# Optimization experiments

Measured on AMD Instinct MI355X. Metric: run time of the kernel, lower is better.

Reference implementation:

```python
import jax, jax.numpy as jnp
import numpy as np

NUM_GROUPS1 = 8
NUM_GROUPS2 = 4
NUM_HEADS = 8


def setup_inputs() -> dict:
    key = jax.random.key(0)
    k1, k2, k3 = jax.random.split(key, 3)
    B, N, C = 8, 4096, 512
    x = jax.random.normal(k1, (B, N, C), dtype=jnp.float32)
    # torch Linear(dim, 3*inner_dim, bias=False); stored transposed for x @ W
    W_qkv = jax.random.normal(k2, (C, 3 * C), dtype=jnp.float32) * 0.02
    W_proj = jax.random.normal(k3, (C, C), dtype=jnp.float32) * 0.02
    b_proj = jnp.zeros((C,), dtype=jnp.float32)
    return {"x": x, "W_qkv": W_qkv, "W_proj": W_proj, "b_proj": b_proj,
            "recursive_index": 0}


def reference(x, W_qkv, W_proj, b_proj, recursive_index):
    # recursive_index is a static Python int (0 -> False branch, num_groups1).
    num_groups = NUM_GROUPS1 if not recursive_index else NUM_GROUPS2
    B, N, C = x.shape
    H = NUM_HEADS
    Dh = C // H
    scale = Dh ** -0.5
    Np = int(np.ceil(N / num_groups) * num_groups)
    if Np != N:
        x = jnp.pad(x, ((0, 0), (0, Np - N), (0, 0)))
    L = Np // num_groups  # tokens per group
    # qkv projection, then split into per-group per-head tensors [B,G,H,L,Dh]
    qkv = (x @ W_qkv).reshape(B, num_groups, L, 3, H, Dh)
    q = jnp.transpose(qkv[:, :, :, 0], (0, 1, 3, 2, 4))
    k = jnp.transpose(qkv[:, :, :, 1], (0, 1, 3, 2, 4))
    v = jnp.transpose(qkv[:, :, :, 2], (0, 1, 3, 2, 4))
    attn = jax.nn.softmax(jnp.einsum('bghld,bghmd->bghlm', q, k) * scale, axis=-1)
    out = jnp.einsum('bghlm,bghmd->bghld', attn, v)  # [B,G,H,L,Dh]
    out = jnp.transpose(out, (0, 1, 3, 2, 4)).reshape(B, Np, C)[:, :N]
    return out @ W_proj + b_proj
```

## Files before the change

### kernel.cpp

```cpp
#include <hip/hip_runtime.h>
#include <hip/hip_bf16.h>

typedef __attribute__((ext_vector_type(8))) short  bf16x8;
typedef __attribute__((ext_vector_type(4))) float  f32x4;

__device__ __forceinline__ ushort f2bf(float f) {
    unsigned u = __builtin_bit_cast(unsigned, f);
    u += 0x7fffu + ((u >> 16) & 1u);
    return (ushort)(u >> 16);
}

__device__ __forceinline__ void gload_lds16(const ushort* g, ushort* l) {
    __builtin_amdgcn_global_load_lds(
        (const __attribute__((address_space(1))) void*)(g),
        (__attribute__((address_space(3))) void*)(l), 16, 0, 0);
}

__global__ __launch_bounds__(256) void cvt_bf16_kernel(
        const float* __restrict__ in, ushort* __restrict__ out, int n4) {
    int i = blockIdx.x * 256 + threadIdx.x;
    if (i >= n4) return;
    float4 f = reinterpret_cast<const float4*>(in)[i];
    ushort4 o;
    o.x = f2bf(f.x); o.y = f2bf(f.y); o.z = f2bf(f.z); o.w = f2bf(f.w);
    reinterpret_cast<ushort4*>(out)[i] = o;
}

__global__ __launch_bounds__(256) void transpose_cvt_kernel(
        const float* __restrict__ in, ushort* __restrict__ out,
        int Cc, int qcols, float qscale) {
    __shared__ ushort t[64 * 65];
    const int cBase = blockIdx.x * 64, rBase = blockIdx.y * 64;
#pragma unroll
    for (int p = 0; p < 16; ++p) {
        int lin = p * 256 + threadIdx.x;
        int r = lin >> 6, c = lin & 63;
        float v = in[(size_t)(rBase + r) * Cc + cBase + c];
        if (cBase + c < qcols) v *= qscale;
        t[c * 65 + r] = f2bf(v);
    }
    __syncthreads();
#pragma unroll
    for (int p = 0; p < 16; ++p) {
        int lin = p * 256 + threadIdx.x;
        int c = lin >> 6, r = lin & 63;
        out[(size_t)(cBase + c) * 512 + rBase + r] = t[c * 65 + r];
    }
}

template<bool F32OUT, bool EMIT_VT>
__global__ __launch_bounds__(256) void gemm_bt_kernel(
        const ushort* __restrict__ A, const ushort* __restrict__ Bt,
        void* __restrict__ Cout, const float* __restrict__ bias,
        ushort* __restrict__ vT, int Ncols, int K) {
    __shared__ ushort smem[8704];
    ushort* la = smem;
    ushort* lb = smem + 4096;
    const int tid  = threadIdx.x;
    const int mBase = blockIdx.y << 7, nBase = blockIdx.x << 7;
    const int w = tid >> 6, lane = tid & 63, ml = lane & 15, quad = lane >> 4;
    const int wr = (w >> 1) << 6, wc = (w & 1) << 6;

    const int srow   = lane >> 2;
    const int schunk = (lane & 3) ^ (srow & 3) ^ ((srow >> 2) & 3);
    const ushort* Ap = A + (size_t)(mBase + w * 32 + srow) * K + schunk * 8;
    const ushort* Bp = Bt + (size_t)(nBase + w * 32 + srow) * K + schunk * 8;
    ushort* lA0 = la + (w * 32) * 32;
    ushort* lB0 = lb + (w * 32) * 32;

    f32x4 z4 = {0.f, 0.f, 0.f, 0.f};
    f32x4 acc[4][4];
#pragma unroll
    for (int i = 0; i < 4; ++i)
#pragma unroll
        for (int j = 0; j < 4; ++j) acc[i][j] = z4;

    const int sx = ((quad ^ (ml & 3) ^ ((ml >> 2) & 3)) << 3);
    const int nkt = K >> 5;
    for (int kt = 0; kt < nkt; ++kt) {
        gload_lds16(Ap,          lA0);
        gload_lds16(Ap + 16 * K, lA0 + 16 * 32);
        gload_lds16(Bp,          lB0);
        gload_lds16(Bp + 16 * K, lB0 + 16 * 32);
        Ap += 32; Bp += 32;
        __syncthreads();
        bf16x8 af[4], bv[4];
#pragma unroll
        for (int i = 0; i < 4; ++i)
            af[i] = *reinterpret_cast<bf16x8*>(la + (wr + i * 16 + ml) * 32 + sx);
#pragma unroll
        for (int j = 0; j < 4; ++j)
            bv[j] = *reinterpret_cast<bf16x8*>(lb + (wc + j * 16 + ml) * 32 + sx);
#pragma unroll
        for (int i = 0; i < 4; ++i)
#pragma unroll
            for (int j = 0; j < 4; ++j)
                acc[i][j] = __builtin_amdgcn_mfma_f32_16x16x32_bf16(af[i], bv[j], acc[i][j], 0, 0, 0);
        __syncthreads();
    }

    if (F32OUT) {
        float* ep = reinterpret_cast<float*>(smem) + w * 1088;
        float bj[4];
#pragma unroll
        for (int j = 0; j < 4; ++j) bj[j] = bias[nBase + wc + j * 16 + ml];
        float* cbase = reinterpret_cast<float*>(Cout);
#pragma unroll
        for (int i = 0; i < 4; ++i) {
#pragma unroll
            for (int j = 0; j < 4; ++j)
#pragma unroll
                for (int r = 0; r < 4; ++r)
                    ep[(quad * 4 + r) * 68 + j * 16 + ml] = acc[i][j][r] + bj[j];
#pragma unroll
            for (int t = 0; t < 4; ++t) {
                int ch = quad + 4 * t;
                float4 v = *reinterpret_cast<const float4*>(ep + ml * 68 + ch * 4);
                *reinterpret_cast<float4*>(cbase
                    + (size_t)(mBase + wr + i * 16 + ml) * Ncols + nBase + wc + ch * 4) = v;
            }
        }
    } else {
        ushort* ep = smem + w * 1152;
        const bool vblk = EMIT_VT && (nBase >= 1024);
#pragma unroll
        for (int i = 0; i < 4; ++i) {
#pragma unroll
            for (int j = 0; j < 4; ++j)
#pragma unroll
                for (int r = 0; r < 4; ++r)
                    ep[(quad * 4 + r) * 72 + j * 16 + ml] = f2bf(acc[i][j][r]);
            if (!vblk) {
#pragma unroll
                for (int t = 0; t < 2; ++t) {
                    int ch = quad + 4 * t;
                    bf16x8 v = *reinterpret_cast<const bf16x8*>(ep + ml * 72 + ch * 8);
                    *reinterpret_cast<bf16x8*>(reinterpret_cast<ushort*>(Cout)
                        + (size_t)(mBase + wr + i * 16 + ml) * Ncols + nBase + wc + ch * 8) = v;
                }
            } else {
#pragma unroll
                for (int t = 0; t < 2; ++t) {
                    bf16x8 p;
#pragma unroll
                    for (int k = 0; k < 8; ++k)
                        p[k] = (short)ep[(t * 8 + k) * 72 + lane];
                    int tok = mBase + wr + i * 16 + t * 8;
                    int vg  = (nBase - 1024) + wc + lane;
                    *reinterpret_cast<bf16x8*>(vT
                        + ((size_t)((tok >> 9) * 512 + vg)) * 512 + (tok & 511)) = p;
                }
            }
        }
    }
}

__global__ __launch_bounds__(256) void attn_kernel(
        const ushort* __restrict__ qk, const ushort* __restrict__ vT,
        ushort* __restrict__ out) {
    __shared__ ushort k_lds[32 * 64];
    __shared__ ushort v_lds[64 * 32];
    __shared__ ushort p_lds[4 * 32 * 40];
    const int tid = threadIdx.x;
    const int w = tid >> 6, lane = tid & 63, ml = lane & 15, quad = lane >> 4;
    const int id = blockIdx.x;
    const int bgh = id >> 2, qc = id & 3;
    const int b = bgh >> 6, g = (bgh >> 3) & 7, h = bgh & 7;
    const int tb = b * 4096 + g * 512;
    const ushort* base  = qk + (size_t)tb * 1024 + h * 64;
    const ushort* vbase = vT + ((size_t)((b * 8 + g) * 512 + h * 64)) * 512;
    const int qOff = qc * 128 + w * 32;

    bf16x8 qf[2][2];
#pragma unroll
    for (int qb = 0; qb < 2; ++qb)
#pragma unroll
        for (int ks = 0; ks < 2; ++ks)
            qf[qb][ks] = *reinterpret_cast<const bf16x8*>(
                base + (size_t)(qOff + qb * 16 + ml) * 1024 + ks * 32 + quad * 8);

    const int krl = lane >> 3;
    const int kch = (lane & 7) ^ krl;
    const ushort* kp = base + (size_t)(w * 8 + krl) * 1024 + 512 + kch * 8;
    ushort* kdst = k_lds + (w * 8) * 64;
    const int vrl = lane >> 2;
    const int vch = (lane & 3) ^ (vrl & 3) ^ ((vrl >> 2) & 3);
    const ushort* vp = vbase + (size_t)(w * 16 + vrl) * 512 + vch * 8;
    ushort* vdst = v_lds + (w * 16) * 32;

    f32x4 z4 = {0.f, 0.f, 0.f, 0.f};
    f32x4 oacc[2][4];
    float lp[2][4];
#pragma unroll
    for (int qb = 0; qb < 2; ++qb) {
#pragma unroll
        for (int db = 0; db < 4; ++db) oacc[qb][db] = z4;
#pragma unroll
        for (int r = 0; r < 4; ++r) lp[qb][r] = 0.f;
    }

    const int ksw = ml & 7;
    const int vsw = (ml & 3) ^ ((ml >> 2) & 3);
    ushort* pw = p_lds + w * 32 * 40;
    for (int kt = 0; kt < 16; ++kt) {
        gload_lds16(kp + (size_t)kt * 32 * 1024, kdst);
        gload_lds16(vp + kt * 32, vdst);
        __syncthreads();

        bf16x8 kf[2][2];
#pragma unroll
        for (int kb = 0; kb < 2; ++kb)
#pragma unroll
            for (int ks = 0; ks < 2; ++ks)
                kf[kb][ks] = *reinterpret_cast<bf16x8*>(
                    k_lds + (kb * 16 + ml) * 64 + (((ks * 4 + quad) ^ ksw) << 3));
        f32x4 s[2][2];
#pragma unroll
        for (int qb = 0; qb < 2; ++qb)
#pragma unroll
            for (int kb = 0; kb < 2; ++kb) {
                f32x4 t = z4;
                t = __builtin_amdgcn_mfma_f32_16x16x32_bf16(qf[qb][0], kf[kb][0], t, 0, 0, 0);
                t = __builtin_amdgcn_mfma_f32_16x16x32_bf16(qf[qb][1], kf[kb][1], t, 0, 0, 0);
                s[qb][kb] = t;
            }

#pragma unroll
        for (int qb = 0; qb < 2; ++qb)
#pragma unroll
            for (int r = 0; r < 4; ++r) {
                float p0 = exp2f(s[qb][0][r]);
                float p1 = exp2f(s[qb][1][r]);
                lp[qb][r] += p0 + p1;
                pw[(qb * 16 + quad * 4 + r) * 40 + ml]      = f2bf(p0);
                pw[(qb * 16 + quad * 4 + r) * 40 + 16 + ml] = f2bf(p1);
            }

        bf16x8 pf[2], vf[4];
#pragma unroll
        for (int qb = 0; qb < 2; ++qb)
            pf[qb] = *reinterpret_cast<bf16x8*>(pw + (qb * 16 + ml) * 40 + quad * 8);
#pragma unroll
        for (int db = 0; db < 4; ++db)
            vf[db] = *reinterpret_cast<bf16x8*>(
                v_lds + (db * 16 + ml) * 32 + ((quad ^ vsw) << 3));
#pragma unroll
        for (int qb = 0; qb < 2; ++qb)
#pragma unroll
            for (int db = 0; db < 4; ++db)
                oacc[qb][db] = __builtin_amdgcn_mfma_f32_16x16x32_bf16(pf[qb], vf[db], oacc[qb][db], 0, 0, 0);
        __syncthreads();
    }

#pragma unroll
    for (int qb = 0; qb < 2; ++qb) {
        float inv[4];
#pragma unroll
        for (int r = 0; r < 4; ++r) {
            float sline = lp[qb][r];
            sline += __shfl_xor(sline, 1);
            sline += __shfl_xor(sline, 2);
            sline += __shfl_xor(sline, 4);
            sline += __shfl_xor(sline, 8);
            inv[r] = 1.0f / sline;
        }
#pragma unroll
        for (int db = 0; db < 4; ++db)
#pragma unroll
            for (int r = 0; r < 4; ++r) {
                float v = oacc[qb][db][r] * inv[r];
                out[(size_t)(tb + qOff + qb * 16 + quad * 4 + r) * 512
                    + h * 64 + db * 16 + ml] = f2bf(v);
            }
    }
}

extern "C" void kernel_launch(void* const* d_in, const int* in_sizes, int n_in,
                              void* d_out, int out_size, void* d_ws, size_t ws_size,
                              hipStream_t stream) {
    const float* x     = (const float*)d_in[0];
    const float* Wqkv  = (const float*)d_in[1];
    const float* Wproj = (const float*)d_in[2];
    const float* bproj = (const float*)d_in[3];

    char* ws = (char*)d_ws;
    ushort* xb   = (ushort*)(ws);
    ushort* wq   = (ushort*)(ws + 33554432);
    ushort* wp   = (ushort*)(ws + 35127296);
    ushort* qkb  = (ushort*)(ws + 35651584);
    ushort* vTb  = (ushort*)(ws + 102760448);
    ushort* attn = xb;
    float*  outp = (float*)d_out;

    cvt_bf16_kernel<<<16384, 256, 0, stream>>>(x, xb, 4194304);
    transpose_cvt_kernel<<<dim3(24, 8), 256, 0, stream>>>(
        Wqkv, wq, 1536, 512, 0.18033688011112043f);
    transpose_cvt_kernel<<<dim3(8, 8), 256, 0, stream>>>(Wproj, wp, 512, 0, 1.0f);
    gemm_bt_kernel<false, true><<<dim3(12, 256), 256, 0, stream>>>(
        xb, wq, qkb, nullptr, vTb, 1024, 512);
    attn_kernel<<<2048, 256, 0, stream>>>(qkb, vTb, attn);
    gemm_bt_kernel<true, false><<<dim3(4, 256), 256, 0, stream>>>(
        attn, wp, outp, bproj, nullptr, 512, 512);
}
```

Measured before the change: 328.0 us.

## Fuse prep kernels, swizzle GEMM tiles, coalesce vT stores, transpose attention scores

Merges the x conversion and both weight transpose/convert launches into one prep kernel, which removes two launches. The GEMM grid becomes 1D with an XCD-aware mapping so neighbouring M tiles share an N column. The V-transpose epilogue now stages a full 64x64 tile in LDS per wave pair and writes contiguous 16-byte token rows instead of scattered 8-element gathers. In attention, the QK MFMA operands are swapped so each lane holds four keys of one query. P can then be stored as packed ushort4 and the row sums need fewer shuffles, at the cost of extra __syncthreads in the vT epilogue.

```diff
diff --git a/kernel.cpp b/kernel.cpp
--- a/kernel.cpp
+++ b/kernel.cpp
@@ -16,35 +16,45 @@
         (__attribute__((address_space(3))) void*)(l), 16, 0, 0);
 }
 
-__global__ __launch_bounds__(256) void cvt_bf16_kernel(
-        const float* __restrict__ in, ushort* __restrict__ out, int n4) {
-    int i = blockIdx.x * 256 + threadIdx.x;
-    if (i >= n4) return;
-    float4 f = reinterpret_cast<const float4*>(in)[i];
-    ushort4 o;
-    o.x = f2bf(f.x); o.y = f2bf(f.y); o.z = f2bf(f.z); o.w = f2bf(f.w);
-    reinterpret_cast<ushort4*>(out)[i] = o;
-}
-
-__global__ __launch_bounds__(256) void transpose_cvt_kernel(
-        const float* __restrict__ in, ushort* __restrict__ out,
-        int Cc, int qcols, float qscale) {
+__global__ __launch_bounds__(256) void prep_kernel(
+        const float* __restrict__ x, ushort* __restrict__ xb,
+        const float* __restrict__ Wqkv, ushort* __restrict__ wq,
+        const float* __restrict__ Wproj, ushort* __restrict__ wp) {
     __shared__ ushort t[64 * 65];
-    const int cBase = blockIdx.x * 64, rBase = blockIdx.y * 64;
+    const int bx = blockIdx.x, tid = threadIdx.x;
+    if (bx < 16384) {
+        int i = bx * 256 + tid;
+        float4 f = reinterpret_cast<const float4*>(x)[i];
+        ushort4 o;
+        o.x = f2bf(f.x); o.y = f2bf(f.y); o.z = f2bf(f.z); o.w = f2bf(f.w);
+        reinterpret_cast<ushort4*>(xb)[i] = o;
+        return;
+    }
+    const float* in; ushort* out; int Cc, qcols, cB, rB; float qs;
+    if (bx < 16576) {
+        int b2 = bx - 16384;
+        in = Wqkv; out = wq; Cc = 1536; qcols = 512;
+        qs = 0.18033688011112043f;
+        cB = (b2 % 24) * 64; rB = (b2 / 24) * 64;
+    } else {
+        int b2 = bx - 16576;
+        in = Wproj; out = wp; Cc = 512; qcols = 0; qs = 1.0f;
+        cB = (b2 % 8) * 64; rB = (b2 / 8) * 64;
+    }
 #pragma unroll
     for (int p = 0; p < 16; ++p) {
-        int lin = p * 256 + threadIdx.x;
+        int lin = p * 256 + tid;
         int r = lin >> 6, c = lin & 63;
-        float v = in[(size_t)(rBase + r) * Cc + cBase + c];
-        if (cBase + c < qcols) v *= qscale;
+        float v = in[(size_t)(rB + r) * Cc + cB + c];
+        if (cB + c < qcols) v *= qs;
         t[c * 65 + r] = f2bf(v);
     }
     __syncthreads();
 #pragma unroll
     for (int p = 0; p < 16; ++p) {
-        int lin = p * 256 + threadIdx.x;
+        int lin = p * 256 + tid;
         int c = lin >> 6, r = lin & 63;
-        out[(size_t)(cBase + c) * 512 + rBase + r] = t[c * 65 + r];
+        out[(size_t)(cB + c) * 512 + rB + r] = t[c * 65 + r];
     }
 }
 
@@ -53,11 +63,13 @@
         const ushort* __restrict__ A, const ushort* __restrict__ Bt,
         void* __restrict__ Cout, const float* __restrict__ bias,
         ushort* __restrict__ vT, int Ncols, int K) {
-    __shared__ ushort smem[8704];
+    __shared__ ushort smem[9216];
     ushort* la = smem;
     ushort* lb = smem + 4096;
     const int tid  = threadIdx.x;
-    const int mBase = blockIdx.y << 7, nBase = blockIdx.x << 7;
+    const int id = blockIdx.x;
+    const int mBase = ((id & 7) * 32 + ((id >> 3) & 31)) << 7;
+    const int nBase = (id >> 8) << 7;
     const int w = tid >> 6, lane = tid & 63, ml = lane & 15, quad = lane >> 4;
     const int wr = (w >> 1) << 6, wc = (w & 1) << 6;
 
@@ -120,9 +132,8 @@
                     + (size_t)(mBase + wr + i * 16 + ml) * Ncols + nBase + wc + ch * 4) = v;
             }
         }
-    } else {
+    } else if (!EMIT_VT || nBase < 1024) {
         ushort* ep = smem + w * 1152;
-        const bool vblk = EMIT_VT && (nBase >= 1024);
 #pragma unroll
         for (int i = 0; i < 4; ++i) {
 #pragma unroll
@@ -130,27 +141,38 @@
 #pragma unroll
                 for (int r = 0; r < 4; ++r)
                     ep[(quad * 4 + r) * 72 + j * 16 + ml] = f2bf(acc[i][j][r]);
-            if (!vblk) {
-#pragma unroll
-                for (int t = 0; t < 2; ++t) {
-                    int ch = quad + 4 * t;
-                    bf16x8 v = *reinterpret_cast<const bf16x8*>(ep + ml * 72 + ch * 8);
-                    *reinterpret_cast<bf16x8*>(reinterpret_cast<ushort*>(Cout)
-                        + (size_t)(mBase + wr + i * 16 + ml) * Ncols + nBase + wc + ch * 8) = v;
+#pragma unroll
+            for (int t = 0; t < 2; ++t) {
+                int ch = quad + 4 * t;
+                bf16x8 v = *reinterpret_cast<const bf16x8*>(ep + ml * 72 + ch * 8);
+                *reinterpret_cast<bf16x8*>(reinterpret_cast<ushort*>(Cout)
+                    + (size_t)(mBase + wr + i * 16 + ml) * Ncols + nBase + wc + ch * 8) = v;
+            }
+        }
+    } else {
+#pragma unroll
+        for (int p = 0; p < 2; ++p) {
+            if ((w >> 1) == p) {
+                ushort* ep = smem + (w & 1) * 4608;
+#pragma unroll
+                for (int i = 0; i < 4; ++i)
+#pragma unroll
+                    for (int j = 0; j < 4; ++j)
+#pragma unroll
+                        for (int r = 0; r < 4; ++r)
+                            ep[(j * 16 + ml) * 72 + i * 16 + quad * 4 + r] = f2bf(acc[i][j][r]);
+                const int tok0 = mBase + wr;
+                const int grp  = tok0 >> 9, tokin = tok0 & 511;
+#pragma unroll
+                for (int pass = 0; pass < 8; ++pass) {
+                    int dl = pass * 8 + (lane >> 3), ch = lane & 7;
+                    bf16x8 v = *reinterpret_cast<const bf16x8*>(ep + dl * 72 + ch * 8);
+                    int vg = (nBase - 1024) + wc + dl;
+                    *reinterpret_cast<bf16x8*>(vT
+                        + ((size_t)(grp * 512 + vg)) * 512 + tokin + ch * 8) = v;
                 }
-            } else {
-#pragma unroll
-                for (int t = 0; t < 2; ++t) {
-                    bf16x8 p;
-#pragma unroll
-                    for (int k = 0; k < 8; ++k)
-                        p[k] = (short)ep[(t * 8 + k) * 72 + lane];
-                    int tok = mBase + wr + i * 16 + t * 8;
-                    int vg  = (nBase - 1024) + wc + lane;
-                    *reinterpret_cast<bf16x8*>(vT
-                        + ((size_t)((tok >> 9) * 512 + vg)) * 512 + (tok & 511)) = p;
-                }
-            }
+            }
+            __syncthreads();
         }
     }
 }
@@ -190,13 +212,12 @@
 
     f32x4 z4 = {0.f, 0.f, 0.f, 0.f};
     f32x4 oacc[2][4];
-    float lp[2][4];
+    float lp[2];
 #pragma unroll
     for (int qb = 0; qb < 2; ++qb) {
 #pragma unroll
         for (int db = 0; db < 4; ++db) oacc[qb][db] = z4;
-#pragma unroll
-        for (int r = 0; r < 4; ++r) lp[qb][r] = 0.f;
+        lp[qb] = 0.f;
     }
 
     const int ksw = ml & 7;
@@ -220,20 +241,22 @@
 #pragma unroll
             for (int kb = 0; kb < 2; ++kb) {
                 f32x4 t = z4;
-                t = __builtin_amdgcn_mfma_f32_16x16x32_bf16(qf[qb][0], kf[kb][0], t, 0, 0, 0);
-                t = __builtin_amdgcn_mfma_f32_16x16x32_bf16(qf[qb][1], kf[kb][1], t, 0, 0, 0);
+                t = __builtin_amdgcn_mfma_f32_16x16x32_bf16(kf[kb][0], qf[qb][0], t, 0, 0, 0);
+                t = __builtin_amdgcn_mfma_f32_16x16x32_bf16(kf[kb][1], qf[qb][1], t, 0, 0, 0);
                 s[qb][kb] = t;
             }
 
 #pragma unroll
         for (int qb = 0; qb < 2; ++qb)
 #pragma unroll
-            for (int r = 0; r < 4; ++r) {
-                float p0 = exp2f(s[qb][0][r]);
-                float p1 = exp2f(s[qb][1][r]);
-                lp[qb][r] += p0 + p1;
-                pw[(qb * 16 + quad * 4 + r) * 40 + ml]      = f2bf(p0);
-                pw[(qb * 16 + quad * 4 + r) * 40 + 16 + ml] = f2bf(p1);
+            for (int kb = 0; kb < 2; ++kb) {
+                float p0 = exp2f(s[qb][kb][0]), p1 = exp2f(s[qb][kb][1]);
+                float p2 = exp2f(s[qb][kb][2]), p3 = exp2f(s[qb][kb][3]);
+                lp[qb] += (p0 + p1) + (p2 + p3);
+                ushort4 pk;
+                pk.x = f2bf(p0); pk.y = f2bf(p1); pk.z = f2bf(p2); pk.w = f2bf(p3);
+                *reinterpret_cast<ushort4*>(
+                    pw + (qb * 16 + ml) * 40 + kb * 16 + quad * 4) = pk;
             }
 
         bf16x8 pf[2], vf[4];
@@ -252,27 +275,27 @@
         __syncthreads();
     }
 
+    float invq[2][4];
 #pragma unroll
     for (int qb = 0; qb < 2; ++qb) {
-        float inv[4];
-#pragma unroll
-        for (int r = 0; r < 4; ++r) {
-            float sline = lp[qb][r];
-            sline += __shfl_xor(sline, 1);
-            sline += __shfl_xor(sline, 2);
-            sline += __shfl_xor(sline, 4);
-            sline += __shfl_xor(sline, 8);
-            inv[r] = 1.0f / sline;
-        }
+        float sline = lp[qb];
+        sline += __shfl_xor(sline, 16);
+        sline += __shfl_xor(sline, 32);
+        float rinv = 1.0f / sline;
+#pragma unroll
+        for (int r = 0; r < 4; ++r)
+            invq[qb][r] = __shfl(rinv, quad * 4 + r);
+    }
+#pragma unroll
+    for (int qb = 0; qb < 2; ++qb)
 #pragma unroll
         for (int db = 0; db < 4; ++db)
 #pragma unroll
             for (int r = 0; r < 4; ++r) {
-                float v = oacc[qb][db][r] * inv[r];
+                float v = oacc[qb][db][r] * invq[qb][r];
                 out[(size_t)(tb + qOff + qb * 16 + quad * 4 + r) * 512
                     + h * 64 + db * 16 + ml] = f2bf(v);
             }
-    }
 }
 
 extern "C" void kernel_launch(void* const* d_in, const int* in_sizes, int n_in,
@@ -292,13 +315,10 @@
     ushort* attn = xb;
     float*  outp = (float*)d_out;
 
-    cvt_bf16_kernel<<<16384, 256, 0, stream>>>(x, xb, 4194304);
-    transpose_cvt_kernel<<<dim3(24, 8), 256, 0, stream>>>(
-        Wqkv, wq, 1536, 512, 0.18033688011112043f);
-    transpose_cvt_kernel<<<dim3(8, 8), 256, 0, stream>>>(Wproj, wp, 512, 0, 1.0f);
-    gemm_bt_kernel<false, true><<<dim3(12, 256), 256, 0, stream>>>(
+    prep_kernel<<<16640, 256, 0, stream>>>(x, xb, Wqkv, wq, Wproj, wp);
+    gemm_bt_kernel<false, true><<<3072, 256, 0, stream>>>(
         xb, wq, qkb, nullptr, vTb, 1024, 512);
     attn_kernel<<<2048, 256, 0, stream>>>(qkb, vTb, attn);
-    gemm_bt_kernel<true, false><<<dim3(4, 256), 256, 0, stream>>>(
+    gemm_bt_kernel<true, false><<<1024, 256, 0, stream>>>(
         attn, wp, outp, bproj, nullptr, 512, 512);
 }
```

Result: faster. 314.8 us (-4.0%).
